# Kernel optimization log

Measured on AMD Instinct MI355X. Metric: run time of the kernel, lower is better.

## Reference

```python
import jax, jax.numpy as jnp
import numpy as np

# ---- Cl(4,1) geometric-product Cayley table (32 blades, metric diag(+,+,+,+,-)) ----
def _build_gp_map():
    metric = [1.0, 1.0, 1.0, 1.0, -1.0]  # e1..e4 square to +1, e5 squares to -1
    gp = np.zeros((32, 32, 32), dtype=np.float32)
    for a in range(32):          # blade a as a bitmask over 5 generators
        for b in range(32):
            # sign from reordering generators into canonical order
            swaps = 0
            t = a >> 1
            while t:
                swaps += bin(t & b).count('1')
                t >>= 1
            sign = -1.0 if (swaps & 1) else 1.0
            # sign from contracted (repeated) generators via the metric
            common = a & b
            for i in range(5):
                if common & (1 << i):
                    sign *= metric[i]
            gp[a, b, a ^ b] = sign  # e_a * e_b = sign * e_{a xor b}
    return gp

GP_MAP = _build_gp_map()  # [32, 32, 32], highly sparse (one nonzero per (a,b))
EPS = 1e-6

B, S, IN, OUT = 2, 1024, 256, 256

def setup_inputs() -> dict:
    key = jax.random.key(0)
    k1, k2 = jax.random.split(key)
    x = jax.random.normal(k1, (B, S, IN, 32), dtype=jnp.float32)
    std = 1.0 / float(np.sqrt(IN * 32))  # grade-aware Xavier scale from reset_parameters
    weight = jax.random.normal(k2, (OUT, IN, 32), dtype=jnp.float32) * std
    return {"x": x, "weight": weight}

def normalize_cl41(mv):
    # normalize each multivector by its coefficient magnitude over the 32 lanes
    norm = jnp.sqrt(jnp.sum(mv * mv, axis=-1, keepdims=True) + EPS)
    return mv / norm

def reference(x, weight):
    gp = jnp.asarray(GP_MAP, dtype=x.dtype)
    # W_op[o,i,l,k] = sum_j weight[o,i,j] * gp[j,l,k]
    W_op = jnp.einsum('oij,jlk->oilk', weight, gp)
    # out[b,s,o,k] = sum_{i,l} x[b,s,i,l] * W_op[o,i,l,k]
    out = jnp.einsum('bsil,oilk->bsok', x, W_op)
    return normalize_cl41(out)
```

## Files before the change

kernel.cpp:

```cpp
#include <hip/hip_runtime.h>
#include <hip/hip_bf16.h>
#include <stdint.h>

typedef _Float16 f16;
typedef __attribute__((ext_vector_type(8))) _Float16 f16x8;
typedef __attribute__((ext_vector_type(4))) float f32x4;

#define M_DIM 2048
#define K_FULL 8192
#define M2 8192
#define K2 2048
#define N2 2048
#define BM 256
#define BN 256
#define BK 64
#define NT (K2 / BK)
#define PSTR 260

struct CMat { int re[4][4]; int im[4][4]; };

constexpr CMat cmul(const CMat& A, const CMat& B) {
  CMat C{};
  for (int r = 0; r < 4; ++r)
    for (int c = 0; c < 4; ++c) {
      int re = 0, im = 0;
      for (int t = 0; t < 4; ++t) {
        re += A.re[r][t] * B.re[t][c] - A.im[r][t] * B.im[t][c];
        im += A.re[r][t] * B.im[t][c] + A.im[r][t] * B.re[t][c];
      }
      C.re[r][c] = re; C.im[r][c] = im;
    }
  return C;
}

constexpr int gp_sign_ct(int a, int b) {
  int sw = 0;
  for (int t = a >> 1; t; t >>= 1) {
    int x = t & b;
    while (x) { sw += x & 1; x >>= 1; }
  }
  int s = (sw & 1) ? -1 : 1;
  if ((a & b) & 16) s = -s;
  return s;
}

struct Tables {
  int8_t f_idx[32][4]; int8_t f_sgn[32][4];
  int8_t g_idx[32][4]; int8_t g_sgn[32][4];
  bool ok;
};

constexpr Tables make_tables() {
  CMat G[5] = {
    { {{0,0,0,1},{0,0,1,0},{0,1,0,0},{1,0,0,0}},
      {{0,0,0,0},{0,0,0,0},{0,0,0,0},{0,0,0,0}} },
    { {{0,0,0,0},{0,0,0,0},{0,0,0,0},{0,0,0,0}},
      {{0,0,0,-1},{0,0,1,0},{0,-1,0,0},{1,0,0,0}} },
    { {{0,0,1,0},{0,0,0,-1},{1,0,0,0},{0,-1,0,0}},
      {{0,0,0,0},{0,0,0,0},{0,0,0,0},{0,0,0,0}} },
    { {{0,0,0,0},{0,0,0,0},{0,0,0,0},{0,0,0,0}},
      {{0,0,-1,0},{0,0,0,-1},{1,0,0,0},{0,1,0,0}} },
    { {{0,0,0,0},{0,0,0,0},{0,0,0,0},{0,0,0,0}},
      {{1,0,0,0},{0,1,0,0},{0,0,-1,0},{0,0,0,-1}} } };
  CMat ID{ {{1,0,0,0},{0,1,0,0},{0,0,1,0},{0,0,0,1}},
           {{0,0,0,0},{0,0,0,0},{0,0,0,0},{0,0,0,0}} };
  CMat U[32] = {};
  for (int A = 0; A < 32; ++A) {
    CMat u = ID;
    for (int b = 0; b < 5; ++b) if (A & (1 << b)) u = cmul(u, G[b]);
    U[A] = u;
  }
  bool ok = true;
  for (int a = 0; a < 32; ++a)
    for (int b = 0; b < 32; ++b) {
      CMat P = cmul(U[a], U[b]);
      int s = gp_sign_ct(a, b);
      const CMat& T = U[a ^ b];
      for (int r = 0; r < 4; ++r)
        for (int c = 0; c < 4; ++c)
          if (P.re[r][c] != s * T.re[r][c] || P.im[r][c] != s * T.im[r][c]) ok = false;
    }
  Tables t{};
  int cnt[32] = {};
  for (int A = 0; A < 32; ++A) {
    int n = 0;
    for (int r = 0; r < 4; ++r)
      for (int c = 0; c < 4; ++c) {
        int vr = U[A].re[r][c], vi = U[A].im[r][c];
        if (vr) {
          int s = (r * 4 + c) * 2;
          if (n < 4 && cnt[s] < 4) {
            t.g_idx[A][n] = (int8_t)s; t.g_sgn[A][n] = (int8_t)vr;
            t.f_idx[s][cnt[s]] = (int8_t)A; t.f_sgn[s][cnt[s]] = (int8_t)vr;
            cnt[s]++;
          } else ok = false;
          n++;
        }
        if (vi) {
          int s = (r * 4 + c) * 2 + 1;
          if (n < 4 && cnt[s] < 4) {
            t.g_idx[A][n] = (int8_t)s; t.g_sgn[A][n] = (int8_t)vi;
            t.f_idx[s][cnt[s]] = (int8_t)A; t.f_sgn[s][cnt[s]] = (int8_t)vi;
            cnt[s]++;
          } else ok = false;
          n++;
        }
      }
    if (n != 4) ok = false;
  }
  for (int s = 0; s < 32; ++s) if (cnt[s] != 4) ok = false;
  t.ok = ok;
  return t;
}

constexpr Tables HT = make_tables();
static_assert(HT.ok, "Cl(4,1) -> M(4,C) homomorphism check FAILED");
static_assert((NT & 1) == 0, "buffer parity requires even tile count");

__device__ __forceinline__ void async16(const f16* g, f16* l) {
  __builtin_amdgcn_global_load_lds(
      (const __attribute__((address_space(1))) uint32_t*)g,
      (__attribute__((address_space(3))) uint32_t*)l,
      16, 0, 0);
}

__device__ __forceinline__ float gp_sign_rt(int a, int b) {
  int sw = 0;
  for (int t = a >> 1; t; t >>= 1) sw += __popc(t & b);
  float s = (sw & 1) ? -1.0f : 1.0f;
  if ((a & b) & 16) s = -s;
  return s;
}

#define FENCE() asm volatile("" ::: "memory")
#define BARRIER() do { FENCE(); __builtin_amdgcn_s_barrier(); FENCE(); } while (0)
#define WAIT_VM(N) asm volatile("s_waitcnt vmcnt(" #N ")" ::: "memory")

__global__ __launch_bounds__(256) void fwd_x_kernel(const float* __restrict__ x,
                                                    f16* __restrict__ Ag) {
  __shared__ float xs[256 * 33];
  const int m = blockIdx.x, t = threadIdx.x;
  const float4* src = (const float4*)(x + (size_t)m * 8192);
#pragma unroll
  for (int c = t; c < 2048; c += 256) {
    float4 v = src[c];
    float* d = xs + (c >> 3) * 33 + ((c & 7) << 2);
    d[0] = v.x; d[1] = v.y; d[2] = v.z; d[3] = v.w;
  }
  __syncthreads();
  const float* xv = xs + t * 33;
  float sv[32];
#pragma unroll
  for (int s = 0; s < 32; ++s)
    sv[s] = (float)HT.f_sgn[s][0] * xv[HT.f_idx[s][0]]
          + (float)HT.f_sgn[s][1] * xv[HT.f_idx[s][1]]
          + (float)HT.f_sgn[s][2] * xv[HT.f_idx[s][2]]
          + (float)HT.f_sgn[s][3] * xv[HT.f_idx[s][3]];
#pragma unroll
  for (int c = 0; c < 4; ++c) {
    f16x8 h;
#pragma unroll
    for (int e = 0; e < 8; ++e) {
      int tt = e >> 1, p = e & 1;
      h[e] = (f16)sv[tt * 8 + c * 2 + p];
    }
    *(f16x8*)(Ag + ((size_t)(m * 4 + c)) * K2 + t * 8) = h;
  }
}

__global__ __launch_bounds__(256) void fwd_w_kernel(const float* __restrict__ w,
                                                    f16* __restrict__ Bt) {
  __shared__ float xs[256 * 33];
  const int o = blockIdx.x, t = threadIdx.x;
  const float4* src = (const float4*)(w + (size_t)o * 8192);
#pragma unroll
  for (int c = t; c < 2048; c += 256) {
    float4 v = src[c];
    float* d = xs + (c >> 3) * 33 + ((c & 7) << 2);
    d[0] = v.x; d[1] = v.y; d[2] = v.z; d[3] = v.w;
  }
  __syncthreads();
  const float* wv = xs + t * 33;
  float sv[32];
#pragma unroll
  for (int s = 0; s < 32; ++s)
    sv[s] = (float)HT.f_sgn[s][0] * wv[HT.f_idx[s][0]]
          + (float)HT.f_sgn[s][1] * wv[HT.f_idx[s][1]]
          + (float)HT.f_sgn[s][2] * wv[HT.f_idx[s][2]]
          + (float)HT.f_sgn[s][3] * wv[HT.f_idx[s][3]];
#pragma unroll
  for (int r = 0; r < 4; ++r)
#pragma unroll
    for (int q = 0; q < 2; ++q) {
      f16x8 h;
#pragma unroll
      for (int e = 0; e < 8; ++e) {
        int tt = e >> 1, p = e & 1;
        float re = sv[(r * 4 + tt) * 2], im = sv[(r * 4 + tt) * 2 + 1];
        float v = (q == 0) ? (p == 0 ? re : -im) : (p == 0 ? im : re);
        h[e] = (f16)v;
      }
      *(f16x8*)(Bt + ((size_t)(o * 8 + r * 2 + q)) * K2 + t * 8) = h;
    }
}

__global__ __launch_bounds__(512, 2) void gemm_fused_kernel(const f16* __restrict__ A,
                                                            const f16* __restrict__ Bw,
                                                            float* __restrict__ out) {
  __shared__ __align__(16) char smem[131072];
  const int t = threadIdx.x;
  const int w = t >> 6, lane = t & 63;
  const int wr = w >> 2, wc = w & 3;
  const int g = lane >> 4, lc = lane & 15;

  const int bid = blockIdx.x;
  const int swzb = (bid & 7) * 32 + (bid >> 3);
  const int by = swzb >> 3, bx = swzb & 7;
  const int m0 = by * BM, n0 = bx * BN;

  const int srow = lane >> 3;
  const int schk = (lane & 7) ^ srow;
  const f16* ga0 = A  + (size_t)(m0 + w * 8 + srow) * K2 + schk * 8;
  const f16* gb0 = Bw + (size_t)(n0 + w * 8 + srow) * K2 + schk * 8;
  const int lw = w << 10;

  const int cks0 = (g ^ (lc & 7)) << 4;
  const int cks1 = ((4 | g) ^ (lc & 7)) << 4;
  const int arow = (wr << 14) + (lc << 7);
  const int brow = 32768 + (wc << 13) + (lc << 7);

  f32x4 acc[8][4];
#pragma unroll
  for (int i = 0; i < 8; ++i)
#pragma unroll
    for (int j = 0; j < 4; ++j) {
      acc[i][j][0] = 0.f; acc[i][j][1] = 0.f; acc[i][j][2] = 0.f; acc[i][j][3] = 0.f;
    }

#define STAGE(bo, kko) do {                                              \
    const int _k = (kko);                                                \
    async16(ga0 + _k,          (f16*)(smem + (bo) + lw));                \
    async16(ga0 + _k + 131072, (f16*)(smem + (bo) + 8192  + lw));        \
    async16(ga0 + _k + 262144, (f16*)(smem + (bo) + 16384 + lw));        \
    async16(ga0 + _k + 393216, (f16*)(smem + (bo) + 24576 + lw));        \
    async16(gb0 + _k,          (f16*)(smem + (bo) + 32768 + lw));        \
    async16(gb0 + _k + 131072, (f16*)(smem + (bo) + 40960 + lw));        \
    async16(gb0 + _k + 262144, (f16*)(smem + (bo) + 49152 + lw));        \
    async16(gb0 + _k + 393216, (f16*)(smem + (bo) + 57344 + lw));        \
  } while (0)

  STAGE(0, 0);
  STAGE(65536, BK);
  WAIT_VM(8);
  BARRIER();

  f16x8 av[4][2], bv[4][2];
  for (int tt = 0; tt < NT; ++tt) {
    const int bo = (tt & 1) << 16;
    const char* ab = smem + bo + arow;
    const char* bb = smem + bo + brow;

#pragma unroll
    for (int i = 0; i < 4; ++i) {
      av[i][0] = *(const f16x8*)(ab + i * 2048 + cks0);
      av[i][1] = *(const f16x8*)(ab + i * 2048 + cks1);
    }
#pragma unroll
    for (int j = 0; j < 2; ++j) {
      bv[j][0] = *(const f16x8*)(bb + j * 2048 + cks0);
      bv[j][1] = *(const f16x8*)(bb + j * 2048 + cks1);
    }
    __builtin_amdgcn_s_setprio(1);
#pragma unroll
    for (int k2 = 0; k2 < 2; ++k2)
#pragma unroll
      for (int i = 0; i < 4; ++i)
#pragma unroll
        for (int j = 0; j < 2; ++j)
          acc[i][j] = __builtin_amdgcn_mfma_f32_16x16x32_f16(av[i][k2], bv[j][k2],
                                                             acc[i][j], 0, 0, 0);
    __builtin_amdgcn_s_setprio(0);
    __builtin_amdgcn_sched_barrier(0);
    BARRIER();

#pragma unroll
    for (int j = 2; j < 4; ++j) {
      bv[j][0] = *(const f16x8*)(bb + j * 2048 + cks0);
      bv[j][1] = *(const f16x8*)(bb + j * 2048 + cks1);
    }
    __builtin_amdgcn_s_setprio(1);
#pragma unroll
    for (int k2 = 0; k2 < 2; ++k2)
#pragma unroll
      for (int i = 0; i < 4; ++i)
#pragma unroll
        for (int j = 2; j < 4; ++j)
          acc[i][j] = __builtin_amdgcn_mfma_f32_16x16x32_f16(av[i][k2], bv[j][k2],
                                                             acc[i][j], 0, 0, 0);
    __builtin_amdgcn_s_setprio(0);
    __builtin_amdgcn_sched_barrier(0);
    BARRIER();

#pragma unroll
    for (int i = 0; i < 4; ++i) {
      av[i][0] = *(const f16x8*)(ab + (4 + i) * 2048 + cks0);
      av[i][1] = *(const f16x8*)(ab + (4 + i) * 2048 + cks1);
    }
    __builtin_amdgcn_s_setprio(1);
#pragma unroll
    for (int k2 = 0; k2 < 2; ++k2)
#pragma unroll
      for (int i = 0; i < 4; ++i)
#pragma unroll
        for (int j = 0; j < 2; ++j)
          acc[4 + i][j] = __builtin_amdgcn_mfma_f32_16x16x32_f16(av[i][k2], bv[j][k2],
                                                                 acc[4 + i][j], 0, 0, 0);
    __builtin_amdgcn_s_setprio(0);
    __builtin_amdgcn_sched_barrier(0);
    BARRIER();

    if (tt + 2 < NT) STAGE(bo, (tt + 2) * BK);
    __builtin_amdgcn_s_setprio(1);
#pragma unroll
    for (int k2 = 0; k2 < 2; ++k2)
#pragma unroll
      for (int i = 0; i < 4; ++i)
#pragma unroll
        for (int j = 2; j < 4; ++j)
          acc[4 + i][j] = __builtin_amdgcn_mfma_f32_16x16x32_f16(av[i][k2], bv[j][k2],
                                                                 acc[4 + i][j], 0, 0, 0);
    __builtin_amdgcn_s_setprio(0);
    __builtin_amdgcn_sched_barrier(0);
    if (tt + 2 < NT) { WAIT_VM(8); }
    else if (tt + 1 < NT) { WAIT_VM(0); }
    BARRIER();
  }
#undef STAGE

  float* ps = (float*)smem;
  __syncthreads();
#pragma unroll
  for (int qq = 0; qq < 4; ++qq) {
    if (qq) __syncthreads();
    if (wr == (qq >> 1)) {
      const int tb = (qq & 1) << 2;
#pragma unroll
      for (int tmi = 0; tmi < 4; ++tmi) {
        const int rowl = tmi * 16 + g * 4;
#pragma unroll
        for (int tn = 0; tn < 4; ++tn) {
          const int col = wc * 64 + tn * 16 + lc;
#pragma unroll
          for (int r = 0; r < 4; ++r)
            ps[(rowl + r) * PSTR + col] = acc[tb + tmi][tn][r];
        }
      }
    }
    __syncthreads();

    const int mh = t >> 5, oh = t & 31;
    float yv[4][8];
#pragma unroll
    for (int c = 0; c < 4; ++c) {
      const float* row = ps + (mh * 4 + c) * PSTR + oh * 8;
      *(float4*)&yv[c][0] = *(const float4*)row;
      *(float4*)&yv[c][4] = *(const float4*)(row + 4);
    }
    float ss = 0.f;
#pragma unroll
    for (int c = 0; c < 4; ++c)
#pragma unroll
      for (int j = 0; j < 8; ++j) ss += yv[c][j] * yv[c][j];
    float inv = rsqrtf(0.25f * ss + 1e-6f);

    float ov[32];
#pragma unroll
    for (int k = 0; k < 32; ++k) {
      float v = 0.f;
#pragma unroll
      for (int j = 0; j < 4; ++j) {
        int s = HT.g_idx[k][j];
        int cell = s >> 1;
        int rr = cell >> 2, cc = cell & 3, pp = s & 1;
        float sgn = (float)HT.g_sgn[k][j];
        v += sgn * yv[cc][rr * 2 + pp];
      }
      ov[k] = v * 0.25f * inv;
    }
    int m = by * 64 + qq * 16 + mh;
    int o = bx * 32 + oh;
    float* op = out + (size_t)m * 8192 + o * 32;
#pragma unroll
    for (int qv = 0; qv < 8; ++qv)
      *(float4*)(op + qv * 4) = make_float4(ov[qv * 4], ov[qv * 4 + 1],
                                            ov[qv * 4 + 2], ov[qv * 4 + 3]);
  }
}

__global__ __launch_bounds__(256) void naive_vl_kernel(const float* __restrict__ x,
                                                       const float* __restrict__ w,
                                                       float* __restrict__ out) {
  __shared__ float xs[8192];
  __shared__ float sgt[1024];
  int m = blockIdx.x, o0 = blockIdx.y << 3;
  int t = threadIdx.x;
  for (int i = t; i < 1024; i += 256) {
    int kk = i >> 5, ll = i & 31;
    sgt[i] = gp_sign_rt(kk ^ ll, ll);
  }
  const float4* xr = (const float4*)(x + (size_t)m * K_FULL);
  float4* xs4 = (float4*)xs;
  for (int i = t; i < 2048; i += 256) xs4[i] = xr[i];
  __syncthreads();
  int k = t & 31, ol = t >> 5;
  int o = o0 + ol;
  const float* wrow = w + (size_t)o * K_FULL;
  float acc = 0.f;
  for (int l = 0; l < 32; ++l) {
    float s = sgt[(k << 5) + l];
    const float* wp = wrow + (k ^ l);
    const float* xp = xs + l;
    float part = 0.f;
#pragma unroll 8
    for (int i = 0; i < 256; ++i) part += xp[i << 5] * wp[i << 5];
    acc += part * s;
  }
  float ss = acc * acc;
  for (int msk = 1; msk < 32; msk <<= 1) ss += __shfl_xor(ss, msk, 32);
  out[((size_t)m * 256 + o) * 32 + k] = acc * rsqrtf(ss + 1e-6f);
}

extern "C" void kernel_launch(void* const* d_in, const int* in_sizes, int n_in,
                              void* d_out, int out_size, void* d_ws, size_t ws_size,
                              hipStream_t stream) {
  const float* x = (const float*)d_in[0];
  const float* w = (const float*)d_in[1];
  float* out = (float*)d_out;

  size_t agE = (size_t)M2 * K2;
  size_t btE = (size_t)N2 * K2;
  size_t need = (agE + btE) * sizeof(f16);

  if (ws_size >= need) {
    f16* Ag = (f16*)d_ws;
    f16* Bt = Ag + agE;
    fwd_x_kernel<<<dim3(M_DIM), dim3(256), 0, stream>>>(x, Ag);
    fwd_w_kernel<<<dim3(256), dim3(256), 0, stream>>>(w, Bt);
    gemm_fused_kernel<<<dim3((M2 / BM) * (N2 / BN)), dim3(512), 0, stream>>>(Ag, Bt, out);
  } else {
    naive_vl_kernel<<<dim3(M_DIM, 32), dim3(256), 0, stream>>>(x, w, out);
  }
}
```

Baseline: 195.5 us.

## Merge prep kernels and interleave next-tile loads across GEMM compute phases

```diff
diff --git a/kernel.cpp b/kernel.cpp
--- a/kernel.cpp
+++ b/kernel.cpp
@@ -135,12 +135,19 @@
 #define FENCE() asm volatile("" ::: "memory")
 #define BARRIER() do { FENCE(); __builtin_amdgcn_s_barrier(); FENCE(); } while (0)
 #define WAIT_VM(N) asm volatile("s_waitcnt vmcnt(" #N ")" ::: "memory")
-
-__global__ __launch_bounds__(256) void fwd_x_kernel(const float* __restrict__ x,
-                                                    f16* __restrict__ Ag) {
+#define LGKM0() do { asm volatile("s_waitcnt lgkmcnt(0)" ::: "memory"); \
+                     __builtin_amdgcn_sched_barrier(0); } while (0)
+
+__global__ __launch_bounds__(256) void fwd_kernel(const float* __restrict__ x,
+                                                  const float* __restrict__ w,
+                                                  f16* __restrict__ Ag,
+                                                  f16* __restrict__ Bt) {
   __shared__ float xs[256 * 33];
-  const int m = blockIdx.x, t = threadIdx.x;
-  const float4* src = (const float4*)(x + (size_t)m * 8192);
+  const int b = blockIdx.x, t = threadIdx.x;
+  const bool isx = (b < M_DIM);
+  const float* src0 = isx ? (x + (size_t)b * 8192)
+                          : (w + (size_t)(b - M_DIM) * 8192);
+  const float4* src = (const float4*)src0;
 #pragma unroll
   for (int c = t; c < 2048; c += 256) {
     float4 v = src[c];
@@ -156,52 +163,34 @@
           + (float)HT.f_sgn[s][1] * xv[HT.f_idx[s][1]]
           + (float)HT.f_sgn[s][2] * xv[HT.f_idx[s][2]]
           + (float)HT.f_sgn[s][3] * xv[HT.f_idx[s][3]];
-#pragma unroll
-  for (int c = 0; c < 4; ++c) {
-    f16x8 h;
-#pragma unroll
-    for (int e = 0; e < 8; ++e) {
-      int tt = e >> 1, p = e & 1;
-      h[e] = (f16)sv[tt * 8 + c * 2 + p];
-    }
-    *(f16x8*)(Ag + ((size_t)(m * 4 + c)) * K2 + t * 8) = h;
-  }
-}
-
-__global__ __launch_bounds__(256) void fwd_w_kernel(const float* __restrict__ w,
-                                                    f16* __restrict__ Bt) {
-  __shared__ float xs[256 * 33];
-  const int o = blockIdx.x, t = threadIdx.x;
-  const float4* src = (const float4*)(w + (size_t)o * 8192);
-#pragma unroll
-  for (int c = t; c < 2048; c += 256) {
-    float4 v = src[c];
-    float* d = xs + (c >> 3) * 33 + ((c & 7) << 2);
-    d[0] = v.x; d[1] = v.y; d[2] = v.z; d[3] = v.w;
-  }
-  __syncthreads();
-  const float* wv = xs + t * 33;
-  float sv[32];
-#pragma unroll
-  for (int s = 0; s < 32; ++s)
-    sv[s] = (float)HT.f_sgn[s][0] * wv[HT.f_idx[s][0]]
-          + (float)HT.f_sgn[s][1] * wv[HT.f_idx[s][1]]
-          + (float)HT.f_sgn[s][2] * wv[HT.f_idx[s][2]]
-          + (float)HT.f_sgn[s][3] * wv[HT.f_idx[s][3]];
-#pragma unroll
-  for (int r = 0; r < 4; ++r)
-#pragma unroll
-    for (int q = 0; q < 2; ++q) {
+  if (isx) {
+#pragma unroll
+    for (int c = 0; c < 4; ++c) {
       f16x8 h;
 #pragma unroll
       for (int e = 0; e < 8; ++e) {
         int tt = e >> 1, p = e & 1;
-        float re = sv[(r * 4 + tt) * 2], im = sv[(r * 4 + tt) * 2 + 1];
-        float v = (q == 0) ? (p == 0 ? re : -im) : (p == 0 ? im : re);
-        h[e] = (f16)v;
-      }
-      *(f16x8*)(Bt + ((size_t)(o * 8 + r * 2 + q)) * K2 + t * 8) = h;
-    }
+        h[e] = (f16)sv[tt * 8 + c * 2 + p];
+      }
+      *(f16x8*)(Ag + ((size_t)(b * 4 + c)) * K2 + t * 8) = h;
+    }
+  } else {
+    const int o = b - M_DIM;
+#pragma unroll
+    for (int r = 0; r < 4; ++r)
+#pragma unroll
+      for (int q = 0; q < 2; ++q) {
+        f16x8 h;
+#pragma unroll
+        for (int e = 0; e < 8; ++e) {
+          int tt = e >> 1, p = e & 1;
+          float re = sv[(r * 4 + tt) * 2], im = sv[(r * 4 + tt) * 2 + 1];
+          float v = (q == 0) ? (p == 0 ? re : -im) : (p == 0 ? im : re);
+          h[e] = (f16)v;
+        }
+        *(f16x8*)(Bt + ((size_t)(o * 8 + r * 2 + q)) * K2 + t * 8) = h;
+      }
+  }
 }
 
 __global__ __launch_bounds__(512, 2) void gemm_fused_kernel(const f16* __restrict__ A,
@@ -237,105 +226,91 @@
       acc[i][j][0] = 0.f; acc[i][j][1] = 0.f; acc[i][j][2] = 0.f; acc[i][j][3] = 0.f;
     }
 
-#define STAGE(bo, kko) do {                                              \
-    const int _k = (kko);                                                \
-    async16(ga0 + _k,          (f16*)(smem + (bo) + lw));                \
-    async16(ga0 + _k + 131072, (f16*)(smem + (bo) + 8192  + lw));        \
-    async16(ga0 + _k + 262144, (f16*)(smem + (bo) + 16384 + lw));        \
-    async16(ga0 + _k + 393216, (f16*)(smem + (bo) + 24576 + lw));        \
-    async16(gb0 + _k,          (f16*)(smem + (bo) + 32768 + lw));        \
-    async16(gb0 + _k + 131072, (f16*)(smem + (bo) + 40960 + lw));        \
-    async16(gb0 + _k + 262144, (f16*)(smem + (bo) + 49152 + lw));        \
-    async16(gb0 + _k + 393216, (f16*)(smem + (bo) + 57344 + lw));        \
+  f16x8 av[4][2], bv[4][2];
+
+#define STG_A(NBO, KK, JB) async16(ga0 + (KK) + (JB) * 131072, \
+                                   (f16*)(smem + (NBO) + (JB) * 8192 + lw))
+#define STG_B(NBO, KK, JB) async16(gb0 + (KK) + (JB) * 131072, \
+                                   (f16*)(smem + (NBO) + 32768 + (JB) * 8192 + lw))
+
+#define RD_A(IO) do {                                                    \
+    _Pragma("unroll")                                                    \
+    for (int i = 0; i < 4; ++i) {                                        \
+      av[i][0] = *(const f16x8*)(ab + ((IO) + i) * 2048 + cks0);         \
+      av[i][1] = *(const f16x8*)(ab + ((IO) + i) * 2048 + cks1);         \
+    } } while (0)
+#define RD_B(J0) do {                                                    \
+    _Pragma("unroll")                                                    \
+    for (int j = 0; j < 2; ++j) {                                        \
+      bv[(J0) + j][0] = *(const f16x8*)(bb + ((J0) + j) * 2048 + cks0);  \
+      bv[(J0) + j][1] = *(const f16x8*)(bb + ((J0) + j) * 2048 + cks1);  \
+    } } while (0)
+
+#define MFMA_Q(IO, J0) do {                                              \
+    __builtin_amdgcn_s_setprio(1);                                       \
+    _Pragma("unroll")                                                    \
+    for (int k2 = 0; k2 < 2; ++k2)                                       \
+      _Pragma("unroll")                                                  \
+      for (int i = 0; i < 4; ++i)                                        \
+        _Pragma("unroll")                                                \
+        for (int j = 0; j < 2; ++j)                                      \
+          acc[(IO) + i][(J0) + j] = __builtin_amdgcn_mfma_f32_16x16x32_f16( \
+              av[i][k2], bv[(J0) + j][k2], acc[(IO) + i][(J0) + j], 0, 0, 0); \
+    __builtin_amdgcn_s_setprio(0);                                       \
+    __builtin_amdgcn_sched_barrier(0);                                   \
   } while (0)
 
-  STAGE(0, 0);
-  STAGE(65536, BK);
-  WAIT_VM(8);
+#define TILE_BODY(U, STG) do {                                           \
+    const int _bo = ((U) & 1) << 16;                                     \
+    const int _nbo = _bo ^ 65536;                                        \
+    const int _kn = ((U) + 1) * BK;                                      \
+    const char* ab = smem + _bo + arow;                                  \
+    const char* bb = smem + _bo + brow;                                  \
+                                                      \
+    RD_A(0); RD_B(0);                                                    \
+    if (STG) { STG_B(_nbo, _kn, 0); STG_B(_nbo, _kn, 1); }               \
+    BARRIER();                                                           \
+    LGKM0();                                                             \
+    MFMA_Q(0, 0);                                                        \
+    BARRIER();                                                           \
+                                                      \
+    RD_B(2);                                                             \
+    if (STG) { STG_B(_nbo, _kn, 2); STG_B(_nbo, _kn, 3); }               \
+    BARRIER();                                                           \
+    if (STG) { WAIT_VM(4); } else { WAIT_VM(0); }                        \
+    LGKM0();                                                             \
+    MFMA_Q(0, 2);                                                        \
+    BARRIER();                                                           \
+                                                      \
+    RD_A(4);                                                             \
+    if (STG) { STG_A(_nbo, _kn, 0); STG_A(_nbo, _kn, 2); }               \
+    BARRIER();                                                           \
+    LGKM0();                                                             \
+    MFMA_Q(4, 0);                                                        \
+    BARRIER();                                                           \
+                                                      \
+    if (STG) { STG_A(_nbo, _kn, 1); STG_A(_nbo, _kn, 3); }               \
+    BARRIER();                                                           \
+    if (STG) { WAIT_VM(2); }                                             \
+    LGKM0();                                                             \
+    MFMA_Q(4, 2);                                                        \
+    BARRIER();                                                           \
+  } while (0)
+
+  STG_B(0, 0, 0); STG_B(0, 0, 1); STG_B(0, 0, 2); STG_B(0, 0, 3);
+  STG_A(0, 0, 0); STG_A(0, 0, 2); STG_A(0, 0, 1); STG_A(0, 0, 3);
+  WAIT_VM(2);
   BARRIER();
 
-  f16x8 av[4][2], bv[4][2];
-  for (int tt = 0; tt < NT; ++tt) {
-    const int bo = (tt & 1) << 16;
-    const char* ab = smem + bo + arow;
-    const char* bb = smem + bo + brow;
-
-#pragma unroll
-    for (int i = 0; i < 4; ++i) {
-      av[i][0] = *(const f16x8*)(ab + i * 2048 + cks0);
-      av[i][1] = *(const f16x8*)(ab + i * 2048 + cks1);
-    }
-#pragma unroll
-    for (int j = 0; j < 2; ++j) {
-      bv[j][0] = *(const f16x8*)(bb + j * 2048 + cks0);
-      bv[j][1] = *(const f16x8*)(bb + j * 2048 + cks1);
-    }
-    __builtin_amdgcn_s_setprio(1);
-#pragma unroll
-    for (int k2 = 0; k2 < 2; ++k2)
-#pragma unroll
-      for (int i = 0; i < 4; ++i)
-#pragma unroll
-        for (int j = 0; j < 2; ++j)
-          acc[i][j] = __builtin_amdgcn_mfma_f32_16x16x32_f16(av[i][k2], bv[j][k2],
-                                                             acc[i][j], 0, 0, 0);
-    __builtin_amdgcn_s_setprio(0);
-    __builtin_amdgcn_sched_barrier(0);
-    BARRIER();
-
-#pragma unroll
-    for (int j = 2; j < 4; ++j) {
-      bv[j][0] = *(const f16x8*)(bb + j * 2048 + cks0);
-      bv[j][1] = *(const f16x8*)(bb + j * 2048 + cks1);
-    }
-    __builtin_amdgcn_s_setprio(1);
-#pragma unroll
-    for (int k2 = 0; k2 < 2; ++k2)
-#pragma unroll
-      for (int i = 0; i < 4; ++i)
-#pragma unroll
-        for (int j = 2; j < 4; ++j)
-          acc[i][j] = __builtin_amdgcn_mfma_f32_16x16x32_f16(av[i][k2], bv[j][k2],
-                                                             acc[i][j], 0, 0, 0);
-    __builtin_amdgcn_s_setprio(0);
-    __builtin_amdgcn_sched_barrier(0);
-    BARRIER();
-
-#pragma unroll
-    for (int i = 0; i < 4; ++i) {
-      av[i][0] = *(const f16x8*)(ab + (4 + i) * 2048 + cks0);
-      av[i][1] = *(const f16x8*)(ab + (4 + i) * 2048 + cks1);
-    }
-    __builtin_amdgcn_s_setprio(1);
-#pragma unroll
-    for (int k2 = 0; k2 < 2; ++k2)
-#pragma unroll
-      for (int i = 0; i < 4; ++i)
-#pragma unroll
-        for (int j = 0; j < 2; ++j)
-          acc[4 + i][j] = __builtin_amdgcn_mfma_f32_16x16x32_f16(av[i][k2], bv[j][k2],
-                                                                 acc[4 + i][j], 0, 0, 0);
-    __builtin_amdgcn_s_setprio(0);
-    __builtin_amdgcn_sched_barrier(0);
-    BARRIER();
-
-    if (tt + 2 < NT) STAGE(bo, (tt + 2) * BK);
-    __builtin_amdgcn_s_setprio(1);
-#pragma unroll
-    for (int k2 = 0; k2 < 2; ++k2)
-#pragma unroll
-      for (int i = 0; i < 4; ++i)
-#pragma unroll
-        for (int j = 2; j < 4; ++j)
-          acc[4 + i][j] = __builtin_amdgcn_mfma_f32_16x16x32_f16(av[i][k2], bv[j][k2],
-                                                                 acc[4 + i][j], 0, 0, 0);
-    __builtin_amdgcn_s_setprio(0);
-    __builtin_amdgcn_sched_barrier(0);
-    if (tt + 2 < NT) { WAIT_VM(8); }
-    else if (tt + 1 < NT) { WAIT_VM(0); }
-    BARRIER();
-  }
-#undef STAGE
+  for (int u = 0; u < NT - 1; ++u) TILE_BODY(u, 1);
+  TILE_BODY(NT - 1, 0);
+
+#undef TILE_BODY
+#undef MFMA_Q
+#undef RD_B
+#undef RD_A
+#undef STG_B
+#undef STG_A
 
   float* ps = (float*)smem;
   __syncthreads();
@@ -444,8 +419,7 @@
   if (ws_size >= need) {
     f16* Ag = (f16*)d_ws;
     f16* Bt = Ag + agE;
-    fwd_x_kernel<<<dim3(M_DIM), dim3(256), 0, stream>>>(x, Ag);
-    fwd_w_kernel<<<dim3(256), dim3(256), 0, stream>>>(w, Bt);
+    fwd_kernel<<<dim3(M_DIM + 256), dim3(256), 0, stream>>>(x, w, Ag, Bt);
     gemm_fused_kernel<<<dim3((M2 / BM) * (N2 / BN)), dim3(512), 0, stream>>>(Ag, Bt, out);
   } else {
     naive_vl_kernel<<<dim3(M_DIM, 32), dim3(256), 0, stream>>>(x, w, out);
```

New measurement: 191.3 us. 2.2% less time.

## Merge preprocessing kernels and restructure GEMM main loop to a single barrier

Applied to the files above, without the earlier changes.

```diff
diff --git a/kernel.cpp b/kernel.cpp
--- a/kernel.cpp
+++ b/kernel.cpp
@@ -136,11 +136,16 @@
 #define BARRIER() do { FENCE(); __builtin_amdgcn_s_barrier(); FENCE(); } while (0)
 #define WAIT_VM(N) asm volatile("s_waitcnt vmcnt(" #N ")" ::: "memory")
 
-__global__ __launch_bounds__(256) void fwd_x_kernel(const float* __restrict__ x,
-                                                    f16* __restrict__ Ag) {
+__global__ __launch_bounds__(256) void fwd_kernel(const float* __restrict__ x,
+                                                  const float* __restrict__ w,
+                                                  f16* __restrict__ Ag,
+                                                  f16* __restrict__ Bt) {
   __shared__ float xs[256 * 33];
-  const int m = blockIdx.x, t = threadIdx.x;
-  const float4* src = (const float4*)(x + (size_t)m * 8192);
+  const int b = blockIdx.x, t = threadIdx.x;
+  const bool isx = (b < M_DIM);
+  const float* src0 = isx ? (x + (size_t)b * 8192)
+                          : (w + (size_t)(b - M_DIM) * 8192);
+  const float4* src = (const float4*)src0;
 #pragma unroll
   for (int c = t; c < 2048; c += 256) {
     float4 v = src[c];
@@ -156,52 +161,34 @@
           + (float)HT.f_sgn[s][1] * xv[HT.f_idx[s][1]]
           + (float)HT.f_sgn[s][2] * xv[HT.f_idx[s][2]]
           + (float)HT.f_sgn[s][3] * xv[HT.f_idx[s][3]];
-#pragma unroll
-  for (int c = 0; c < 4; ++c) {
-    f16x8 h;
-#pragma unroll
-    for (int e = 0; e < 8; ++e) {
-      int tt = e >> 1, p = e & 1;
-      h[e] = (f16)sv[tt * 8 + c * 2 + p];
-    }
-    *(f16x8*)(Ag + ((size_t)(m * 4 + c)) * K2 + t * 8) = h;
-  }
-}
-
-__global__ __launch_bounds__(256) void fwd_w_kernel(const float* __restrict__ w,
-                                                    f16* __restrict__ Bt) {
-  __shared__ float xs[256 * 33];
-  const int o = blockIdx.x, t = threadIdx.x;
-  const float4* src = (const float4*)(w + (size_t)o * 8192);
-#pragma unroll
-  for (int c = t; c < 2048; c += 256) {
-    float4 v = src[c];
-    float* d = xs + (c >> 3) * 33 + ((c & 7) << 2);
-    d[0] = v.x; d[1] = v.y; d[2] = v.z; d[3] = v.w;
-  }
-  __syncthreads();
-  const float* wv = xs + t * 33;
-  float sv[32];
-#pragma unroll
-  for (int s = 0; s < 32; ++s)
-    sv[s] = (float)HT.f_sgn[s][0] * wv[HT.f_idx[s][0]]
-          + (float)HT.f_sgn[s][1] * wv[HT.f_idx[s][1]]
-          + (float)HT.f_sgn[s][2] * wv[HT.f_idx[s][2]]
-          + (float)HT.f_sgn[s][3] * wv[HT.f_idx[s][3]];
-#pragma unroll
-  for (int r = 0; r < 4; ++r)
-#pragma unroll
-    for (int q = 0; q < 2; ++q) {
+  if (isx) {
+#pragma unroll
+    for (int c = 0; c < 4; ++c) {
       f16x8 h;
 #pragma unroll
       for (int e = 0; e < 8; ++e) {
         int tt = e >> 1, p = e & 1;
-        float re = sv[(r * 4 + tt) * 2], im = sv[(r * 4 + tt) * 2 + 1];
-        float v = (q == 0) ? (p == 0 ? re : -im) : (p == 0 ? im : re);
-        h[e] = (f16)v;
-      }
-      *(f16x8*)(Bt + ((size_t)(o * 8 + r * 2 + q)) * K2 + t * 8) = h;
-    }
+        h[e] = (f16)sv[tt * 8 + c * 2 + p];
+      }
+      *(f16x8*)(Ag + ((size_t)(b * 4 + c)) * K2 + t * 8) = h;
+    }
+  } else {
+    const int o = b - M_DIM;
+#pragma unroll
+    for (int r = 0; r < 4; ++r)
+#pragma unroll
+      for (int q = 0; q < 2; ++q) {
+        f16x8 h;
+#pragma unroll
+        for (int e = 0; e < 8; ++e) {
+          int tt = e >> 1, p = e & 1;
+          float re = sv[(r * 4 + tt) * 2], im = sv[(r * 4 + tt) * 2 + 1];
+          float v = (q == 0) ? (p == 0 ? re : -im) : (p == 0 ? im : re);
+          h[e] = (f16)v;
+        }
+        *(f16x8*)(Bt + ((size_t)(o * 8 + r * 2 + q)) * K2 + t * 8) = h;
+      }
+  }
 }
 
 __global__ __launch_bounds__(512, 2) void gemm_fused_kernel(const f16* __restrict__ A,
@@ -237,39 +224,41 @@
       acc[i][j][0] = 0.f; acc[i][j][1] = 0.f; acc[i][j][2] = 0.f; acc[i][j][3] = 0.f;
     }
 
-#define STAGE(bo, kko) do {                                              \
-    const int _k = (kko);                                                \
-    async16(ga0 + _k,          (f16*)(smem + (bo) + lw));                \
-    async16(ga0 + _k + 131072, (f16*)(smem + (bo) + 8192  + lw));        \
-    async16(ga0 + _k + 262144, (f16*)(smem + (bo) + 16384 + lw));        \
-    async16(ga0 + _k + 393216, (f16*)(smem + (bo) + 24576 + lw));        \
-    async16(gb0 + _k,          (f16*)(smem + (bo) + 32768 + lw));        \
-    async16(gb0 + _k + 131072, (f16*)(smem + (bo) + 40960 + lw));        \
-    async16(gb0 + _k + 262144, (f16*)(smem + (bo) + 49152 + lw));        \
-    async16(gb0 + _k + 393216, (f16*)(smem + (bo) + 57344 + lw));        \
-  } while (0)
-
-  STAGE(0, 0);
-  STAGE(65536, BK);
-  WAIT_VM(8);
+  f16x8 avA[4][2], avB[4][2], bvA[2][2], bvB[2][2];
+
+#define STG_A(NBO, KK, JB) async16(ga0 + (KK) + (JB) * 131072, \
+                                   (f16*)(smem + (NBO) + (JB) * 8192 + lw))
+#define STG_B(NBO, KK, JB) async16(gb0 + (KK) + (JB) * 131072, \
+                                   (f16*)(smem + (NBO) + 32768 + (JB) * 8192 + lw))
+
+  STG_A(0, 0, 0); STG_A(0, 0, 1); STG_A(0, 0, 2); STG_A(0, 0, 3);
+  STG_B(0, 0, 0); STG_B(0, 0, 1); STG_B(0, 0, 2); STG_B(0, 0, 3);
+  WAIT_VM(0);
   BARRIER();
 
-  f16x8 av[4][2], bv[4][2];
-  for (int tt = 0; tt < NT; ++tt) {
-    const int bo = (tt & 1) << 16;
+#pragma unroll 2
+  for (int u = 0; u < NT; ++u) {
+    const int bo = (u & 1) << 16;
+    const int nbo = bo ^ 65536;
+    const int kn = (u + 1) * BK;
     const char* ab = smem + bo + arow;
     const char* bb = smem + bo + brow;
-
-#pragma unroll
-    for (int i = 0; i < 4; ++i) {
-      av[i][0] = *(const f16x8*)(ab + i * 2048 + cks0);
-      av[i][1] = *(const f16x8*)(ab + i * 2048 + cks1);
-    }
-#pragma unroll
-    for (int j = 0; j < 2; ++j) {
-      bv[j][0] = *(const f16x8*)(bb + j * 2048 + cks0);
-      bv[j][1] = *(const f16x8*)(bb + j * 2048 + cks1);
-    }
+    const bool stg = (u + 1 < NT);
+
+#pragma unroll
+    for (int i = 0; i < 4; ++i) avA[i][0] = *(const f16x8*)(ab + i * 2048 + cks0);
+#pragma unroll
+    for (int j = 0; j < 2; ++j) bvA[j][0] = *(const f16x8*)(bb + j * 2048 + cks0);
+#pragma unroll
+    for (int i = 0; i < 4; ++i) avA[i][1] = *(const f16x8*)(ab + i * 2048 + cks1);
+#pragma unroll
+    for (int j = 0; j < 2; ++j) bvA[j][1] = *(const f16x8*)(bb + j * 2048 + cks1);
+
+    if (stg) {
+      STG_A(nbo, kn, 0); STG_A(nbo, kn, 1); STG_A(nbo, kn, 2); STG_A(nbo, kn, 3);
+      STG_B(nbo, kn, 0); STG_B(nbo, kn, 1); STG_B(nbo, kn, 2); STG_B(nbo, kn, 3);
+    }
+
     __builtin_amdgcn_s_setprio(1);
 #pragma unroll
     for (int k2 = 0; k2 < 2; ++k2)
@@ -277,35 +266,32 @@
       for (int i = 0; i < 4; ++i)
 #pragma unroll
         for (int j = 0; j < 2; ++j)
-          acc[i][j] = __builtin_amdgcn_mfma_f32_16x16x32_f16(av[i][k2], bv[j][k2],
+          acc[i][j] = __builtin_amdgcn_mfma_f32_16x16x32_f16(avA[i][k2], bvA[j][k2],
                                                              acc[i][j], 0, 0, 0);
     __builtin_amdgcn_s_setprio(0);
-    __builtin_amdgcn_sched_barrier(0);
-    BARRIER();
-
-#pragma unroll
-    for (int j = 2; j < 4; ++j) {
-      bv[j][0] = *(const f16x8*)(bb + j * 2048 + cks0);
-      bv[j][1] = *(const f16x8*)(bb + j * 2048 + cks1);
-    }
+
+#pragma unroll
+    for (int j = 0; j < 2; ++j) {
+      bvB[j][0] = *(const f16x8*)(bb + (2 + j) * 2048 + cks0);
+      bvB[j][1] = *(const f16x8*)(bb + (2 + j) * 2048 + cks1);
+    }
+#pragma unroll
+    for (int i = 0; i < 4; ++i) {
+      avB[i][0] = *(const f16x8*)(ab + (4 + i) * 2048 + cks0);
+      avB[i][1] = *(const f16x8*)(ab + (4 + i) * 2048 + cks1);
+    }
+
     __builtin_amdgcn_s_setprio(1);
 #pragma unroll
     for (int k2 = 0; k2 < 2; ++k2)
 #pragma unroll
       for (int i = 0; i < 4; ++i)
 #pragma unroll
-        for (int j = 2; j < 4; ++j)
-          acc[i][j] = __builtin_amdgcn_mfma_f32_16x16x32_f16(av[i][k2], bv[j][k2],
-                                                             acc[i][j], 0, 0, 0);
+        for (int j = 0; j < 2; ++j)
+          acc[i][2 + j] = __builtin_amdgcn_mfma_f32_16x16x32_f16(avA[i][k2], bvB[j][k2],
+                                                                 acc[i][2 + j], 0, 0, 0);
     __builtin_amdgcn_s_setprio(0);
-    __builtin_amdgcn_sched_barrier(0);
-    BARRIER();
-
-#pragma unroll
-    for (int i = 0; i < 4; ++i) {
-      av[i][0] = *(const f16x8*)(ab + (4 + i) * 2048 + cks0);
-      av[i][1] = *(const f16x8*)(ab + (4 + i) * 2048 + cks1);
-    }
+
     __builtin_amdgcn_s_setprio(1);
 #pragma unroll
     for (int k2 = 0; k2 < 2; ++k2)
@@ -313,29 +299,29 @@
       for (int i = 0; i < 4; ++i)
 #pragma unroll
         for (int j = 0; j < 2; ++j)
-          acc[4 + i][j] = __builtin_amdgcn_mfma_f32_16x16x32_f16(av[i][k2], bv[j][k2],
+          acc[4 + i][j] = __builtin_amdgcn_mfma_f32_16x16x32_f16(avB[i][k2], bvA[j][k2],
                                                                  acc[4 + i][j], 0, 0, 0);
     __builtin_amdgcn_s_setprio(0);
-    __builtin_amdgcn_sched_barrier(0);
-    BARRIER();
-
-    if (tt + 2 < NT) STAGE(bo, (tt + 2) * BK);
+
     __builtin_amdgcn_s_setprio(1);
 #pragma unroll
     for (int k2 = 0; k2 < 2; ++k2)
 #pragma unroll
       for (int i = 0; i < 4; ++i)
 #pragma unroll
-        for (int j = 2; j < 4; ++j)
-          acc[4 + i][j] = __builtin_amdgcn_mfma_f32_16x16x32_f16(av[i][k2], bv[j][k2],
-                                                                 acc[4 + i][j], 0, 0, 0);
+        for (int j = 0; j < 2; ++j)
+          acc[4 + i][2 + j] = __builtin_amdgcn_mfma_f32_16x16x32_f16(avB[i][k2], bvB[j][k2],
+                                                                     acc[4 + i][2 + j], 0, 0, 0);
     __builtin_amdgcn_s_setprio(0);
-    __builtin_amdgcn_sched_barrier(0);
-    if (tt + 2 < NT) { WAIT_VM(8); }
-    else if (tt + 1 < NT) { WAIT_VM(0); }
-    BARRIER();
-  }
-#undef STAGE
+
+    if (stg) {
+      WAIT_VM(0);
+      BARRIER();
+    }
+  }
+
+#undef STG_B
+#undef STG_A
 
   float* ps = (float*)smem;
   __syncthreads();
@@ -444,8 +430,7 @@
   if (ws_size >= need) {
     f16* Ag = (f16*)d_ws;
     f16* Bt = Ag + agE;
-    fwd_x_kernel<<<dim3(M_DIM), dim3(256), 0, stream>>>(x, Ag);
-    fwd_w_kernel<<<dim3(256), dim3(256), 0, stream>>>(w, Bt);
+    fwd_kernel<<<dim3(M_DIM + 256), dim3(256), 0, stream>>>(x, w, Ag, Bt);
     gemm_fused_kernel<<<dim3((M2 / BM) * (N2 / BN)), dim3(512), 0, stream>>>(Ag, Bt, out);
   } else {
     naive_vl_kernel<<<dim3(M_DIM, 32), dim3(256), 0, stream>>>(x, w, out);
```

Result: faster. 191.3 us (-2.2%).
